# Kernel tuning notes

Hardware: AMD Instinct MI355X
Metric: run time of the kernel (lower is better)

Reference implementation:

```python
import jax, jax.numpy as jnp
import numpy as np

DIM = 512
HEADS = 8
DIM_HEAD = 64  # dim // 8
LANDMARKS = 256  # dim // 2
PINV_ITERS = 6
CONV_K = 33  # residual_conv_kernel default in nystrom-attention
SCALE = DIM_HEAD ** -0.5


def setup_inputs() -> dict:
    key = jax.random.key(0)
    ks = jax.random.split(key, 6)
    B, N = 4, 4096
    inner = HEADS * DIM_HEAD  # 512
    x = jax.random.normal(ks[0], (B, N, DIM), dtype=jnp.float32)
    gamma = jnp.ones((DIM,), jnp.float32)
    beta = jnp.zeros((DIM,), jnp.float32)
    w_qkv = jax.random.normal(ks[1], (DIM, 3 * inner), jnp.float32) * 0.02
    w_out = jax.random.normal(ks[2], (inner, DIM), jnp.float32) * 0.02
    b_out = jnp.zeros((DIM,), jnp.float32)
    # depthwise Conv2d(heads, heads, (33,1), groups=heads, bias=False): OIHW = (H,1,33,1)
    conv_w = jax.random.normal(ks[3], (HEADS, 1, CONV_K, 1), jnp.float32) * 0.1
    return {"x": x, "gamma": gamma, "beta": beta, "w_qkv": w_qkv,
            "w_out": w_out, "b_out": b_out, "conv_w": conv_w}


def _layernorm(x, gamma, beta, eps=1e-5):
    mu = x.mean(-1, keepdims=True)
    var = ((x - mu) ** 2).mean(-1, keepdims=True)
    return (x - mu) * jax.lax.rsqrt(var + eps) * gamma + beta


def _pinv_newton_schulz(a, iters=PINV_ITERS):
    # Moore-Penrose pseudo-inverse via iterative scheme (lucidrains)
    abs_a = jnp.abs(a)
    col = abs_a.sum(-1).max()  # global scalar max, as torch.max
    row = abs_a.sum(-2).max()
    z = jnp.swapaxes(a, -1, -2) / (col * row)
    I = jnp.eye(a.shape[-1], dtype=a.dtype)
    for _ in range(iters):
        az = a @ z
        z = 0.25 * z @ (13. * I - az @ (15. * I - az @ (7. * I - az)))
    return z


def reference(x, gamma, beta, w_qkv, w_out, b_out, conv_w):
    B, N, _ = x.shape
    m = LANDMARKS
    l = N // m  # N chosen divisible by m, so no padding branch
    xn = _layernorm(x, gamma, beta)
    qkv = xn @ w_qkv  # [B,N,3*inner]
    q, k, v = jnp.split(qkv, 3, axis=-1)
    # [B,H,N,D]
    def split_heads(t):
        return t.reshape(B, N, HEADS, DIM_HEAD).transpose(0, 2, 1, 3)
    q, k, v = split_heads(q) * SCALE, split_heads(k), split_heads(v)
    # landmarks: mean over contiguous groups of l tokens -> [B,H,m,D]
    q_l = q.reshape(B, HEADS, m, l, DIM_HEAD).mean(3)
    k_l = k.reshape(B, HEADS, m, l, DIM_HEAD).mean(3)
    attn1 = jax.nn.softmax(jnp.einsum('bhid,bhjd->bhij', q, k_l), axis=-1)    # [B,H,N,m]
    attn2 = jax.nn.softmax(jnp.einsum('bhid,bhjd->bhij', q_l, k_l), axis=-1)  # [B,H,m,m]
    attn3 = jax.nn.softmax(jnp.einsum('bhid,bhjd->bhij', q_l, k), axis=-1)    # [B,H,m,N]
    attn2_inv = _pinv_newton_schulz(attn2)
    out = (attn1 @ attn2_inv) @ (attn3 @ v)  # [B,H,N,D]
    # residual depthwise conv over sequence dim, per head (channels=heads)
    out = out + jax.lax.conv_general_dilated(
        v, conv_w, window_strides=(1, 1),
        padding=[(CONV_K // 2, CONV_K // 2), (0, 0)],
        dimension_numbers=('NCHW', 'OIHW', 'NCHW'),
        feature_group_count=HEADS)
    out = out.transpose(0, 2, 1, 3).reshape(B, N, HEADS * DIM_HEAD)
    attn_out = out @ w_out + b_out  # dropout is identity at eval
    return x + attn_out
```

## Files before the change

### kernel.cpp

```cpp
#include <hip/hip_runtime.h>
#include <math.h>

#define BH 32
#define N_ 4096
#define D_ 64
#define M_ 256
#define L_ 16
#define DIM_ 512
#define K3_ 1536

typedef __attribute__((ext_vector_type(4))) float f32x4;
typedef __attribute__((ext_vector_type(8))) short s16x8;
typedef unsigned short ushort_t;

__device__ inline ushort_t f2bf(float f){
  union{float f; unsigned u;} v; v.f = f;
  unsigned r = v.u + 0x7fffu + ((v.u >> 16) & 1u);
  return (ushort_t)(r >> 16);
}
__device__ inline float bf2f(ushort_t b){
  union{unsigned u; float f;} v; v.u = ((unsigned)b) << 16; return v.f;
}

__device__ inline void gl_lds16(const ushort_t* g, ushort_t* l){
  __builtin_amdgcn_global_load_lds(
      (const __attribute__((address_space(1))) unsigned int*)g,
      (__attribute__((address_space(3))) unsigned int*)l, 16, 0, 0);
}

__device__ inline int xcd_swz_bid(){
  int bid = blockIdx.x + gridDim.x*(blockIdx.y + gridDim.y*blockIdx.z);
  int nwg = gridDim.x*gridDim.y*gridDim.z;
  int cpx = nwg >> 3;
  return (bid & 7)*cpx + (bid >> 3);
}

__device__ inline float wave_sum(float v){
  #pragma unroll
  for (int o=32;o;o>>=1) v += __shfl_down(v,o,64);
  return v;
}
__device__ inline float wave_max(float v){
  #pragma unroll
  for (int o=32;o;o>>=1) v = fmaxf(v,__shfl_down(v,o,64));
  return v;
}
__device__ inline float blk_sum256(float v, float* sm){
  v = wave_sum(v);
  int lane = threadIdx.x & 63, wid = threadIdx.x >> 6;
  if (lane==0) sm[wid]=v;
  __syncthreads();
  float r = sm[0]+sm[1]+sm[2]+sm[3];
  __syncthreads();
  return r;
}
__device__ inline float blk_max256(float v, float* sm){
  v = wave_max(v);
  int lane = threadIdx.x & 63, wid = threadIdx.x >> 6;
  if (lane==0) sm[wid]=v;
  __syncthreads();
  float r = fmaxf(fmaxf(sm[0],sm[1]),fmaxf(sm[2],sm[3]));
  __syncthreads();
  return r;
}

__global__ __launch_bounds__(256) void ln_k(const float* __restrict__ x,
    const float* __restrict__ g, const float* __restrict__ bt, ushort_t* __restrict__ xn){
  int row = blockIdx.x, t = threadIdx.x;
  __shared__ float sm[4];
  const float* xr = x + (size_t)row*DIM_;
  float v0 = xr[t], v1 = xr[t+256];
  float mu = blk_sum256(v0+v1, sm) * (1.f/DIM_);
  float d0 = v0-mu, d1 = v1-mu;
  float var = blk_sum256(d0*d0+d1*d1, sm) * (1.f/DIM_);
  float rs = rsqrtf(var + 1e-5f);
  ushort_t* xo = xn + (size_t)row*DIM_;
  xo[t]     = f2bf(d0*rs*g[t]     + bt[t]);
  xo[t+256] = f2bf(d1*rs*g[t+256] + bt[t+256]);
}

__global__ __launch_bounds__(256) void twb_k(const float* __restrict__ src,
    ushort_t* __restrict__ dst, int R, int C){
  __shared__ ushort_t tile[64][66];
  size_t boff = (size_t)blockIdx.z * R * C;
  int r0 = blockIdx.y*64, c0 = blockIdx.x*64;
  int t = threadIdx.x, c = t & 63, r4 = t >> 6;
  #pragma unroll
  for (int i=0;i<16;i++){
    int rr = r4 + i*4;
    tile[c][rr] = f2bf(src[boff + (size_t)(r0+rr)*C + (c0+c)]);
  }
  __syncthreads();
  #pragma unroll
  for (int i=0;i<16;i++){
    int cc = r4 + i*4;
    dst[boff + (size_t)(c0+cc)*R + (r0 + c)] = tile[cc][c];
  }
}
__global__ __launch_bounds__(256) void tbb_k(const ushort_t* __restrict__ src,
    ushort_t* __restrict__ dst, int R, int C){
  __shared__ ushort_t tile[64][66];
  size_t boff = (size_t)blockIdx.z * R * C;
  int r0 = blockIdx.y*64, c0 = blockIdx.x*64;
  int t = threadIdx.x, c = t & 63, r4 = t >> 6;
  #pragma unroll
  for (int i=0;i<16;i++){
    int rr = r4 + i*4;
    tile[c][rr] = src[boff + (size_t)(r0+rr)*C + (c0+c)];
  }
  __syncthreads();
  #pragma unroll
  for (int i=0;i<16;i++){
    int cc = r4 + i*4;
    dst[boff + (size_t)(c0+cc)*R + (r0 + c)] = tile[cc][c];
  }
}

__global__ __launch_bounds__(256) void gemm_qkv_k(const ushort_t* __restrict__ A,
    const ushort_t* __restrict__ Bt, ushort_t* __restrict__ qb, ushort_t* __restrict__ kb,
    ushort_t* __restrict__ vb){
  __shared__ __align__(16) ushort_t As[128*64];
  __shared__ __align__(16) ushort_t Bs[128*64];
  int t = threadIdx.x;
  int lane = t & 63, wave = t >> 6;
  int l16 = lane & 15, quad = lane >> 4;
  int wm = (wave & 1) * 64, wn = (wave >> 1) * 64;
  int swz = xcd_swz_bid();
  int bx = swz % gridDim.x, by = swz / gridDim.x;
  int row0 = by * 128, col0 = bx * 128;
  f32x4 acc[4][4];
  #pragma unroll
  for (int i=0;i<4;i++)
    #pragma unroll
    for (int j=0;j<4;j++) acc[i][j] = (f32x4){0.f,0.f,0.f,0.f};
  int lr = lane >> 3, lc = lane & 7;
  int scol = (lc ^ lr) * 8;
  int rx7 = l16 & 7;
  for (int k0=0;k0<DIM_;k0+=64){
    __syncthreads();
    #pragma unroll
    for (int p=0;p<4;p++){
      int r = wave*8 + p*32;
      gl_lds16(&A [(size_t)(row0+r+lr)*DIM_ + k0 + scol], &As[(size_t)r*64]);
      gl_lds16(&Bt[(size_t)(col0+r+lr)*DIM_ + k0 + scol], &Bs[(size_t)r*64]);
    }
    __syncthreads();
    s16x8 af[4][2], bf[4][2];
    #pragma unroll
    for (int mt=0;mt<4;mt++)
      #pragma unroll
      for (int kk=0;kk<2;kk++)
        af[mt][kk] = *(const s16x8*)&As[(wm + mt*16 + l16)*64 + (((kk*4+quad)^rx7)*8)];
    #pragma unroll
    for (int nt=0;nt<4;nt++)
      #pragma unroll
      for (int kk=0;kk<2;kk++)
        bf[nt][kk] = *(const s16x8*)&Bs[(wn + nt*16 + l16)*64 + (((kk*4+quad)^rx7)*8)];
    #pragma unroll
    for (int mt=0;mt<4;mt++)
      #pragma unroll
      for (int nt=0;nt<4;nt++)
        #pragma unroll
        for (int kk=0;kk<2;kk++)
          acc[mt][nt] = __builtin_amdgcn_mfma_f32_16x16x32_bf16(af[mt][kk], bf[nt][kk], acc[mt][nt], 0,0,0);
  }
  #pragma unroll
  for (int mt=0;mt<4;mt++){
    #pragma unroll
    for (int nt=0;nt<4;nt++){
      #pragma unroll
      for (int reg=0;reg<4;reg++){
        int row = row0 + wm + mt*16 + quad*4 + reg;
        int col = col0 + wn + nt*16 + l16;
        float val = acc[mt][nt][reg];
        int b = row >> 12, n = row & 4095;
        int which = col >> 9, rem = col & 511;
        int h = rem >> 6, d = rem & 63;
        size_t dst = ((size_t)((b<<3)+h)*N_ + n)*D_ + d;
        if (which==0)      qb[dst] = f2bf(val*0.125f);
        else if (which==1) kb[dst] = f2bf(val);
        else               vb[dst] = f2bf(val);
      }
    }
  }
}

__global__ __launch_bounds__(256) void final3_k(const ushort_t* __restrict__ A,
    const ushort_t* __restrict__ Bt, const float* __restrict__ bo,
    const float* __restrict__ x, float* __restrict__ y){
  __shared__ __align__(16) ushort_t As[128*64];
  __shared__ __align__(16) ushort_t Bs[64*64];
  int t = threadIdx.x;
  int lane = t & 63, wave = t >> 6;
  int l16 = lane & 15, quad = lane >> 4;
  int wm = wave * 32;
  int swz = xcd_swz_bid();
  int bx = swz % gridDim.x, by = swz / gridDim.x;
  int row0 = by * 128, col0 = bx * 64;
  f32x4 acc[2][4];
  #pragma unroll
  for (int i=0;i<2;i++)
    #pragma unroll
    for (int j=0;j<4;j++) acc[i][j] = (f32x4){0.f,0.f,0.f,0.f};
  int lr = lane >> 3, lc = lane & 7;
  int scol = (lc ^ lr) * 8;
  int rx7 = l16 & 7;
  for (int k0=0;k0<DIM_;k0+=64){
    __syncthreads();
    #pragma unroll
    for (int p=0;p<4;p++){
      int r = wave*8 + p*32;
      gl_lds16(&A[(size_t)(row0+r+lr)*DIM_ + k0 + scol], &As[(size_t)r*64]);
    }
    #pragma unroll
    for (int p=0;p<2;p++){
      int r = wave*8 + p*32;
      gl_lds16(&Bt[(size_t)(col0+r+lr)*DIM_ + k0 + scol], &Bs[(size_t)r*64]);
    }
    __syncthreads();
    s16x8 af[2][2], bf[4][2];
    #pragma unroll
    for (int mt=0;mt<2;mt++)
      #pragma unroll
      for (int kk=0;kk<2;kk++)
        af[mt][kk] = *(const s16x8*)&As[(wm + mt*16 + l16)*64 + (((kk*4+quad)^rx7)*8)];
    #pragma unroll
    for (int nt=0;nt<4;nt++)
      #pragma unroll
      for (int kk=0;kk<2;kk++)
        bf[nt][kk] = *(const s16x8*)&Bs[(nt*16 + l16)*64 + (((kk*4+quad)^rx7)*8)];
    #pragma unroll
    for (int mt=0;mt<2;mt++)
      #pragma unroll
      for (int nt=0;nt<4;nt++)
        #pragma unroll
        for (int kk=0;kk<2;kk++)
          acc[mt][nt] = __builtin_amdgcn_mfma_f32_16x16x32_bf16(af[mt][kk], bf[nt][kk], acc[mt][nt], 0,0,0);
  }
  #pragma unroll
  for (int mt=0;mt<2;mt++){
    #pragma unroll
    for (int nt=0;nt<4;nt++){
      int col = col0 + nt*16 + l16;
      #pragma unroll
      for (int reg=0;reg<4;reg++){
        int row = row0 + wm + mt*16 + quad*4 + reg;
        size_t o = (size_t)row*DIM_ + col;
        y[o] = acc[mt][nt][reg] + bo[col] + x[o];
      }
    }
  }
}

__global__ void lmk_k(const ushort_t* __restrict__ q, const ushort_t* __restrict__ k,
                      float* __restrict__ ql, float* __restrict__ kl,
                      ushort_t* __restrict__ qlh, ushort_t* __restrict__ qll,
                      ushort_t* __restrict__ klh, ushort_t* __restrict__ kll){
  int idx = blockIdx.x*256 + threadIdx.x;
  int d = idx & 63, i = (idx >> 6) & 255, bh = idx >> 14;
  size_t base = ((size_t)bh*N_ + i*L_)*D_ + d;
  float sq=0.f, sk=0.f;
  #pragma unroll
  for (int tt=0;tt<L_;tt++){ sq += bf2f(q[base + (size_t)tt*D_]); sk += bf2f(k[base + (size_t)tt*D_]); }
  sq *= (1.f/L_); sk *= (1.f/L_);
  ql[idx] = sq; kl[idx] = sk;
  ushort_t qh = f2bf(sq), kh = f2bf(sk);
  qlh[idx] = qh; qll[idx] = f2bf(sq - bf2f(qh));
  klh[idx] = kh; kll[idx] = f2bf(sk - bf2f(kh));
}

__global__ __launch_bounds__(256) void attn2m_k(
    const ushort_t* __restrict__ qlh, const ushort_t* __restrict__ qll,
    const ushort_t* __restrict__ klh, const ushort_t* __restrict__ kll,
    float* __restrict__ a2f, ushort_t* __restrict__ a2h, ushort_t* __restrict__ a2l,
    float* __restrict__ cs, float* __restrict__ rs){
  int bh = blockIdx.y;
  int t = threadIdx.x, wave = t >> 6, lane = t & 63;
  int l16 = lane & 15, quad = lane >> 4;
  size_t mo = (size_t)bh*M_*M_;
  int rowtile = blockIdx.x*32 + wave*16;
  size_t qbase = ((size_t)bh*M_ + rowtile + l16)*D_;
  s16x8 qh0 = *(const s16x8*)&qlh[qbase + quad*8];
  s16x8 qh1 = *(const s16x8*)&qlh[qbase + 32 + quad*8];
  s16x8 qv0 = *(const s16x8*)&qll[qbase + quad*8];
  s16x8 qv1 = *(const s16x8*)&qll[qbase + 32 + quad*8];
  f32x4 s[16];
  #pragma unroll
  for (int kt=0;kt<16;kt++){
    size_t kb = ((size_t)bh*M_ + kt*16 + l16)*D_;
    s16x8 kh0 = *(const s16x8*)&klh[kb + quad*8];
    s16x8 kh1 = *(const s16x8*)&klh[kb + 32 + quad*8];
    s16x8 kv0 = *(const s16x8*)&kll[kb + quad*8];
    s16x8 kv1 = *(const s16x8*)&kll[kb + 32 + quad*8];
    f32x4 z = (f32x4){0.f,0.f,0.f,0.f};
    z = __builtin_amdgcn_mfma_f32_16x16x32_bf16(qh0, kh0, z, 0,0,0);
    z = __builtin_amdgcn_mfma_f32_16x16x32_bf16(qh1, kh1, z, 0,0,0);
    z = __builtin_amdgcn_mfma_f32_16x16x32_bf16(qh0, kv0, z, 0,0,0);
    z = __builtin_amdgcn_mfma_f32_16x16x32_bf16(qh1, kv1, z, 0,0,0);
    z = __builtin_amdgcn_mfma_f32_16x16x32_bf16(qv0, kh0, z, 0,0,0);
    z = __builtin_amdgcn_mfma_f32_16x16x32_bf16(qv1, kh1, z, 0,0,0);
    s[kt] = z;
  }
  float mx[4], inv[4];
  #pragma unroll
  for (int r=0;r<4;r++){
    float m = s[0][r];
    #pragma unroll
    for (int kt=1;kt<16;kt++) m = fmaxf(m, s[kt][r]);
    m = fmaxf(m, __shfl_xor(m, 1));
    m = fmaxf(m, __shfl_xor(m, 2));
    m = fmaxf(m, __shfl_xor(m, 4));
    m = fmaxf(m, __shfl_xor(m, 8));
    mx[r] = m;
  }
  float lsum[4] = {0.f,0.f,0.f,0.f};
  #pragma unroll
  for (int kt=0;kt<16;kt++){
    #pragma unroll
    for (int r=0;r<4;r++){
      float e = expf(s[kt][r] - mx[r]);
      s[kt][r] = e;
      lsum[r] += e;
    }
  }
  #pragma unroll
  for (int r=0;r<4;r++){
    float ls = lsum[r];
    ls += __shfl_xor(ls, 1);
    ls += __shfl_xor(ls, 2);
    ls += __shfl_xor(ls, 4);
    ls += __shfl_xor(ls, 8);
    inv[r] = 1.f/ls;
  }
  if (l16 == 0){
    #pragma unroll
    for (int r=0;r<4;r++) rs[(size_t)bh*M_ + rowtile + quad*4 + r] = 1.0f;
  }
  #pragma unroll
  for (int kt=0;kt<16;kt++){
    int c = kt*16 + l16;
    float csum = 0.f;
    #pragma unroll
    for (int r=0;r<4;r++){
      float p = s[kt][r]*inv[r];
      csum += p;
      size_t oi = mo + (size_t)(rowtile + quad*4 + r)*M_ + c;
      a2f[oi] = p;
      ushort_t hh = f2bf(p);
      a2h[oi] = hh;
      a2l[oi] = f2bf(p - bf2f(hh));
    }
    csum += __shfl_xor(csum, 16);
    csum += __shfl_xor(csum, 32);
    if (lane < 16) atomicAdd(&cs[(size_t)bh*M_ + c], csum);
  }
}

__global__ __launch_bounds__(256) void maxred_k(const float* __restrict__ cs,
    const float* __restrict__ rs, float* __restrict__ scal){
  __shared__ float sm[4];
  float cm=-1e30f, rm=-1e30f;
  for (int i=threadIdx.x;i<BH*M_;i+=256){ cm=fmaxf(cm,cs[i]); rm=fmaxf(rm,rs[i]); }
  cm = blk_max256(cm, sm);
  rm = blk_max256(rm, sm);
  if (threadIdx.x==0) scal[0] = 1.f/(cm*rm);
}

__global__ __launch_bounds__(256) void initz3_k(const float* __restrict__ a2,
    const float* __restrict__ scal,
    ushort_t* __restrict__ zh, ushort_t* __restrict__ zl,
    ushort_t* __restrict__ zTh, ushort_t* __restrict__ zTl){
  __shared__ float tile[64][65];
  int bh = blockIdx.z;
  size_t mo = (size_t)bh*M_*M_;
  float s = scal[0];
  int r0 = blockIdx.y*64, c0 = blockIdx.x*64;
  int t = threadIdx.x, c = t & 63, r4 = t >> 6;
  #pragma unroll
  for (int i=0;i<16;i++){
    int rr = r4 + i*4;
    float v = a2[mo + (size_t)(r0+rr)*M_ + c0 + c] * s;
    tile[rr][c] = v;
    ushort_t hh = f2bf(v);
    size_t oi = mo + (size_t)(r0+rr)*M_ + c0 + c;
    zTh[oi] = hh;
    zTl[oi] = f2bf(v - bf2f(hh));
  }
  __syncthreads();
  #pragma unroll
  for (int i=0;i<16;i++){
    int zr = r4 + i*4;
    float v = tile[c][zr];
    size_t oi = mo + (size_t)(c0+zr)*M_ + r0 + c;
    ushort_t hh = f2bf(v);
    zh[oi] = hh;
    zl[oi] = f2bf(v - bf2f(hh));
  }
}

template<bool HASCOEF, bool WN, bool WT, bool WF>
__global__ __launch_bounds__(256) void ns3_k(
    const ushort_t* __restrict__ Ah, const ushort_t* __restrict__ Al,
    const ushort_t* __restrict__ BTh, const ushort_t* __restrict__ BTl,
    float coef, float scale,
    ushort_t* __restrict__ Ch, ushort_t* __restrict__ Cl,
    ushort_t* __restrict__ CTh, ushort_t* __restrict__ CTl,
    float* __restrict__ Cf){
  __shared__ __align__(16) ushort_t Ahs[64*64];
  __shared__ __align__(16) ushort_t Als[64*64];
  __shared__ __align__(16) ushort_t Bhs[64*64];
  __shared__ __align__(16) ushort_t Bls[64*64];
  int swz = xcd_swz_bid();
  int bx = swz % gridDim.x; int rem = swz / gridDim.x;
  int by = rem % gridDim.y; int batch = rem / gridDim.y;
  size_t mo = (size_t)batch*M_*M_;
  int row0 = by*64, col0 = bx*64;
  int t = threadIdx.x, lane = t & 63, wave = t >> 6;
  int l16 = lane & 15, quad = lane >> 4;
  f32x4 acc[4];
  #pragma unroll
  for (int j=0;j<4;j++) acc[j] = (f32x4){0.f,0.f,0.f,0.f};
  int lr = lane >> 3, lc = lane & 7;
  int scol = (lc ^ lr) * 8;
  int rx7 = l16 & 7;
  for (int k0=0;k0<M_;k0+=64){
    __syncthreads();
    #pragma unroll
    for (int p=0;p<2;p++){
      int r = wave*8 + p*32;
      gl_lds16(&Ah [mo + (size_t)(row0+r+lr)*M_ + k0 + scol], &Ahs[(size_t)r*64]);
      gl_lds16(&Al [mo + (size_t)(row0+r+lr)*M_ + k0 + scol], &Als[(size_t)r*64]);
      gl_lds16(&BTh[mo + (size_t)(col0+r+lr)*M_ + k0 + scol], &Bhs[(size_t)r*64]);
      gl_lds16(&BTl[mo + (size_t)(col0+r+lr)*M_ + k0 + scol], &Bls[(size_t)r*64]);
    }
    __syncthreads();
    s16x8 fah[2], fal[2];
    #pragma unroll
    for (int kk=0;kk<2;kk++){
      fah[kk] = *(const s16x8*)&Ahs[(wave*16 + l16)*64 + (((kk*4+quad)^rx7)*8)];
      fal[kk] = *(const s16x8*)&Als[(wave*16 + l16)*64 + (((kk*4+quad)^rx7)*8)];
    }
    #pragma unroll
    for (int nt=0;nt<4;nt++){
      #pragma unroll
      for (int kk=0;kk<2;kk++){
        s16x8 fbh = *(const s16x8*)&Bhs[(nt*16 + l16)*64 + (((kk*4+quad)^rx7)*8)];
        s16x8 fbl = *(const s16x8*)&Bls[(nt*16 + l16)*64 + (((kk*4+quad)^rx7)*8)];
        acc[nt] = __builtin_amdgcn_mfma_f32_16x16x32_bf16(fah[kk], fbh, acc[nt], 0,0,0);
        acc[nt] = __builtin_amdgcn_mfma_f32_16x16x32_bf16(fah[kk], fbl, acc[nt], 0,0,0);
        acc[nt] = __builtin_amdgcn_mfma_f32_16x16x32_bf16(fal[kk], fbh, acc[nt], 0,0,0);
      }
    }
  }
  int rbase = row0 + wave*16 + quad*4;
  #pragma unroll
  for (int nt=0;nt<4;nt++){
    int c = col0 + nt*16 + l16;
    ushort_t th[4], tl[4];
    #pragma unroll
    for (int reg=0;reg<4;reg++){
      float a = acc[nt][reg];
      float base = 0.f;
      if (HASCOEF){
        size_t ai = mo + (size_t)(rbase+reg)*M_ + c;
        base = coef*(bf2f(Ah[ai]) + bf2f(Al[ai]));
      }
      float v = scale*(base - a);
      if (WF) Cf[mo + (size_t)(rbase+reg)*M_ + c] = v;
      ushort_t hh = f2bf(v);
      ushort_t ll = f2bf(v - bf2f(hh));
      if (WN){
        Ch[mo + (size_t)(rbase+reg)*M_ + c] = hh;
        Cl[mo + (size_t)(rbase+reg)*M_ + c] = ll;
      }
      th[reg] = hh; tl[reg] = ll;
    }
    if (WT){
      uint2 vh; vh.x = (unsigned)th[0] | ((unsigned)th[1]<<16); vh.y = (unsigned)th[2] | ((unsigned)th[3]<<16);
      uint2 vl; vl.x = (unsigned)tl[0] | ((unsigned)tl[1]<<16); vl.y = (unsigned)tl[2] | ((unsigned)tl[3]<<16);
      *(uint2*)&CTh[mo + (size_t)c*M_ + rbase] = vh;
      *(uint2*)&CTl[mo + (size_t)c*M_ + rbase] = vl;
    }
  }
}

template<int ITERS, bool SCATTER>
__global__ __launch_bounds__(256) void attn7_k(const ushort_t* __restrict__ Q,
    const ushort_t* __restrict__ K, const ushort_t* __restrict__ VT,
    int nq, int nk,
    float* __restrict__ up, float* __restrict__ mst, float* __restrict__ lst,
    ushort_t* __restrict__ ob){
  __shared__ __align__(16) ushort_t Ks[64*72];
  __shared__ __align__(16) ushort_t Vs[64*72];
  __shared__ __align__(16) ushort_t Pb[4*16*76];
  int swz = xcd_swz_bid();
  int qblk = swz % gridDim.x; int rem0 = swz / gridDim.x;
  int half = rem0 % gridDim.y; int bh = rem0 / gridDim.y;
  int key0 = half * (ITERS*64);
  int t = threadIdx.x, wave = t >> 6, lane = t & 63;
  int l16 = lane & 15, quad = lane >> 4;
  size_t qbase = ((size_t)bh*nq + qblk*64 + wave*16 + l16)*D_;
  s16x8 qa0 = *(const s16x8*)&Q[qbase + quad*8];
  s16x8 qa1 = *(const s16x8*)&Q[qbase + 32 + quad*8];
  const ushort_t* Kb = K + (size_t)bh*nk*D_;
  const ushort_t* Vb = VT + (size_t)bh*D_*nk;
  ushort_t* Pw = &Pb[wave*16*76];
  float m_j = -1e30f, l_j = 0.f;
  f32x4 oacc[4];
  #pragma unroll
  for (int d=0;d<4;d++) oacc[d] = (f32x4){0.f,0.f,0.f,0.f};
  for (int it=0; it<ITERS; it++){
    int j0 = key0 + it*64;
    __syncthreads();
    #pragma unroll
    for (int p=0;p<2;p++){
      int idx = t + p*256;
      int kr = idx >> 3, kc = (idx & 7)*8;
      *(uint4*)&Ks[kr*72 + kc] = *(const uint4*)&Kb[(size_t)(j0+kr)*D_ + kc];
      *(uint4*)&Vs[kr*72 + kc] = *(const uint4*)&Vb[(size_t)kr*nk + j0 + kc];
    }
    __syncthreads();
    f32x4 st[4];
    #pragma unroll
    for (int kt=0;kt<4;kt++){
      s16x8 b0 = *(const s16x8*)&Ks[(kt*16 + l16)*72 + quad*8];
      s16x8 b1 = *(const s16x8*)&Ks[(kt*16 + l16)*72 + 32 + quad*8];
      f32x4 z = (f32x4){0.f,0.f,0.f,0.f};
      z = __builtin_amdgcn_mfma_f32_16x16x32_bf16(b0, qa0, z, 0,0,0);
      z = __builtin_amdgcn_mfma_f32_16x16x32_bf16(b1, qa1, z, 0,0,0);
      st[kt] = z;
    }
    float mx = st[0][0];
    #pragma unroll
    for (int kt=0;kt<4;kt++)
      #pragma unroll
      for (int r=0;r<4;r++) mx = fmaxf(mx, st[kt][r]);
    mx = fmaxf(mx, __shfl_xor(mx, 16));
    mx = fmaxf(mx, __shfl_xor(mx, 32));
    float mn = fmaxf(m_j, mx);
    float alpha = __expf(m_j - mn);
    m_j = mn;
    float lsum = 0.f;
    #pragma unroll
    for (int kt=0;kt<4;kt++){
      ushort_t pk[4];
      #pragma unroll
      for (int r=0;r<4;r++){
        float p = __expf(st[kt][r] - mn);
        lsum += p;
        pk[r] = f2bf(p);
      }
      uint2 w;
      w.x = (unsigned)pk[0] | ((unsigned)pk[1] << 16);
      w.y = (unsigned)pk[2] | ((unsigned)pk[3] << 16);
      *(uint2*)&Pw[l16*76 + kt*16 + quad*4] = w;
    }
    lsum += __shfl_xor(lsum, 16);
    lsum += __shfl_xor(lsum, 32);
    l_j = l_j*alpha + lsum;
    float ab[4];
    #pragma unroll
    for (int r=0;r<4;r++) ab[r] = __shfl(alpha, quad*4 + r, 64);
    #pragma unroll
    for (int d=0;d<4;d++)
      #pragma unroll
      for (int r=0;r<4;r++) oacc[d][r] *= ab[r];
    #pragma unroll
    for (int ks=0;ks<2;ks++){
      s16x8 pa = *(const s16x8*)&Pw[l16*76 + ks*32 + quad*8];
      #pragma unroll
      for (int dt=0;dt<4;dt++){
        s16x8 vv = *(const s16x8*)&Vs[(dt*16 + l16)*72 + ks*32 + quad*8];
        oacc[dt] = __builtin_amdgcn_mfma_f32_16x16x32_bf16(pa, vv, oacc[dt], 0,0,0);
      }
    }
  }
  int rowbase = qblk*64 + wave*16 + quad*4;
  if (SCATTER){
    float lb[4];
    #pragma unroll
    for (int r=0;r<4;r++) lb[r] = __shfl(l_j, quad*4 + r, 64);
    int b = bh >> 3, h = bh & 7;
    #pragma unroll
    for (int dt=0;dt<4;dt++){
      #pragma unroll
      for (int r=0;r<4;r++){
        int n = rowbase + r;
        ob[((size_t)(b*N_ + n))*DIM_ + h*D_ + dt*16 + l16] = f2bf(oacc[dt][r] / lb[r]);
      }
    }
  } else {
    size_t pb = ((size_t)(half*BH + bh)*M_ + rowbase)*D_;
    #pragma unroll
    for (int dt=0;dt<4;dt++){
      #pragma unroll
      for (int r=0;r<4;r++)
        up[pb + (size_t)r*D_ + dt*16 + l16] = oacc[dt][r];
    }
    if (lane < 16){
      size_t si = (size_t)(half*BH + bh)*M_ + qblk*64 + wave*16 + l16;
      mst[si] = m_j;
      lst[si] = l_j;
    }
  }
}

__global__ __launch_bounds__(256) void comb_k(const float* __restrict__ up,
    const float* __restrict__ mst, const float* __restrict__ lst,
    float* __restrict__ u){
  int idx = blockIdx.x*256 + threadIdx.x;
  int d = idx & 63; int row = (idx >> 6) & 255; int bh = idx >> 14;
  float m = -1e30f;
  float mv[8];
  #pragma unroll
  for (int hfs=0;hfs<8;hfs++){
    mv[hfs] = mst[(size_t)(hfs*BH + bh)*M_ + row];
    m = fmaxf(m, mv[hfs]);
  }
  float num = 0.f, den = 0.f;
  #pragma unroll
  for (int hfs=0;hfs<8;hfs++){
    float w = __expf(mv[hfs] - m);
    size_t ri = (size_t)(hfs*BH + bh)*M_ + row;
    den += lst[ri] * w;
    num += up[ri*D_ + d] * w;
  }
  u[idx] = num / den;
}

__global__ void zu_k(const float* __restrict__ z, const float* __restrict__ u,
                     float* __restrict__ w){
  int idx = blockIdx.x*256 + threadIdx.x;
  int d = idx & 63, i = (idx >> 6) & 255, bh = idx >> 14;
  const float* zr = z + ((size_t)bh*M_+i)*M_;
  const float* ub = u + (size_t)bh*M_*D_ + d;
  float acc = 0.f;
  for (int kk=0;kk<M_;kk++) acc += zr[kk]*ub[(size_t)kk*D_];
  w[idx] = acc;
}

__global__ __launch_bounds__(256) void conv3_k(const ushort_t* __restrict__ v,
    const float* __restrict__ cw, ushort_t* __restrict__ ob){
  int bh = blockIdx.y;
  int h = bh & 7, b = bh >> 3;
  int t = threadIdx.x;
  int d8 = (t & 7) * 8;
  int nloc = t >> 3;
  int n0 = blockIdx.x * 128 + nloc * 4;
  __shared__ float wsm[33];
  if (t < 33) wsm[t] = cw[h*33 + t];
  __syncthreads();
  float acc[4][8];
  #pragma unroll
  for (int j=0;j<4;j++)
    #pragma unroll
    for (int dd=0;dd<8;dd++) acc[j][dd] = 0.f;
  const ushort_t* vbase = v + (size_t)bh*N_*D_;
  for (int r=0;r<36;r++){
    int nn = n0 - 16 + r;
    float vals[8];
    if (nn >= 0 && nn < N_){
      uint4 raw = *(const uint4*)&vbase[(size_t)nn*D_ + d8];
      const ushort_t* pr = (const ushort_t*)&raw;
      #pragma unroll
      for (int dd=0;dd<8;dd++) vals[dd] = bf2f(pr[dd]);
    } else {
      #pragma unroll
      for (int dd=0;dd<8;dd++) vals[dd] = 0.f;
    }
    #pragma unroll
    for (int j=0;j<4;j++){
      int tap = r - j;
      if (tap >= 0 && tap <= 32){
        float wj = wsm[tap];
        #pragma unroll
        for (int dd=0;dd<8;dd++) acc[j][dd] += wj * vals[dd];
      }
    }
  }
  #pragma unroll
  for (int j=0;j<4;j++){
    size_t oi = ((size_t)(b*N_ + n0 + j))*DIM_ + h*D_ + d8;
    uint4 cur = *(uint4*)&ob[oi];
    ushort_t* pc = (ushort_t*)&cur;
    #pragma unroll
    for (int dd=0;dd<8;dd++) pc[dd] = f2bf(bf2f(pc[dd]) + acc[j][dd]);
    *(uint4*)&ob[oi] = cur;
  }
}

extern "C" void kernel_launch(void* const* d_in, const int* in_sizes, int n_in,
                              void* d_out, int out_size, void* d_ws, size_t ws_size,
                              hipStream_t stream){
  (void)in_sizes; (void)n_in; (void)out_size; (void)ws_size;
  const float* x      = (const float*)d_in[0];
  const float* gamma  = (const float*)d_in[1];
  const float* beta   = (const float*)d_in[2];
  const float* w_qkv  = (const float*)d_in[3];
  const float* w_out  = (const float*)d_in[4];
  const float* b_out  = (const float*)d_in[5];
  const float* conv_w = (const float*)d_in[6];
  float* y = (float*)d_out;
  float* ws = (float*)d_ws;

  size_t off = 0;
  ushort_t* xnb   = (ushort_t*)(ws + off); off += 4194304;
  ushort_t* qb    = (ushort_t*)(ws + off); off += 4194304;
  ushort_t* kb    = (ushort_t*)(ws + off); off += 4194304;
  ushort_t* vb    = (ushort_t*)(ws + off); off += 4194304;
  ushort_t* vT    = (ushort_t*)(ws + off); off += 4194304;
  ushort_t* wqkvT = (ushort_t*)(ws + off); off += 393216;
  ushort_t* woutT = (ushort_t*)(ws + off); off += 131072;
  ushort_t* qlh   = (ushort_t*)(ws + off); off += 262144;
  ushort_t* qll   = (ushort_t*)(ws + off); off += 262144;
  ushort_t* klh   = (ushort_t*)(ws + off); off += 262144;
  ushort_t* kll   = (ushort_t*)(ws + off); off += 262144;
  ushort_t* wzT   = (ushort_t*)(ws + off); off += 262144;
  ushort_t* ob    = (ushort_t*)(ws + off); off += 4194304;
  ushort_t* a2h   = (ushort_t*)(ws + off); off += 1048576;
  ushort_t* a2l   = (ushort_t*)(ws + off); off += 1048576;
  ushort_t* z0h   = (ushort_t*)(ws + off); off += 1048576;
  ushort_t* z0l   = (ushort_t*)(ws + off); off += 1048576;
  ushort_t* z0Th  = (ushort_t*)(ws + off); off += 1048576;
  ushort_t* z0Tl  = (ushort_t*)(ws + off); off += 1048576;
  ushort_t* z1h   = (ushort_t*)(ws + off); off += 1048576;
  ushort_t* z1l   = (ushort_t*)(ws + off); off += 1048576;
  ushort_t* z1Th  = (ushort_t*)(ws + off); off += 1048576;
  ushort_t* z1Tl  = (ushort_t*)(ws + off); off += 1048576;
  ushort_t* t1Th  = (ushort_t*)(ws + off); off += 1048576;
  ushort_t* t1Tl  = (ushort_t*)(ws + off); off += 1048576;
  ushort_t* t2Th  = (ushort_t*)(ws + off); off += 1048576;
  ushort_t* t2Tl  = (ushort_t*)(ws + off); off += 1048576;
  float* ql  = ws + off;  off += 524288;
  float* kl  = ws + off;  off += 524288;
  float* a2f = ws + off;  off += 2097152;
  float* zf  = ws + off;  off += 2097152;
  float* u   = ws + off;  off += 524288;
  float* wz  = ws + off;  off += 524288;
  float* up  = ws + off;  off += 4194304;
  float* mstat = ws + off; off += 65536;
  float* lstat = ws + off; off += 65536;
  float* cs  = ws + off;  off += 8192;
  float* rs  = ws + off;  off += 8192;
  float* scal = ws + off; off += 8;
  ushort_t* azh  = xnb;
  ushort_t* azl  = xnb + 2097152;
  ushort_t* azTh = xnb + 2*2097152;
  ushort_t* azTl = xnb + 3*2097152;

  hipMemsetAsync(cs, 0, BH*M_*sizeof(float), stream);
  ln_k<<<16384,256,0,stream>>>(x, gamma, beta, xnb);
  twb_k<<<dim3(24,8,1),256,0,stream>>>(w_qkv, wqkvT, 512, 1536);
  twb_k<<<dim3(8,8,1),256,0,stream>>>(w_out, woutT, 512, 512);
  gemm_qkv_k<<<dim3(12,128),256,0,stream>>>(xnb, wqkvT, qb, kb, vb);
  tbb_k<<<dim3(1,64,32),256,0,stream>>>(vb, vT, 4096, 64);
  lmk_k<<<2048,256,0,stream>>>(qb, kb, ql, kl, qlh, qll, klh, kll);
  attn2m_k<<<dim3(8,32),128,0,stream>>>(qlh, qll, klh, kll, a2f, a2h, a2l, cs, rs);
  maxred_k<<<1,256,0,stream>>>(cs, rs, scal);
  initz3_k<<<dim3(4,4,32),256,0,stream>>>(a2f, scal, z0h, z0l, z0Th, z0Tl);

  ushort_t *zch = z0h, *zcl = z0l, *zcTh = z0Th, *zcTl = z0Tl;
  ushort_t *znh = z1h, *znl = z1l, *znTh = z1Th, *znTl = z1Tl;
  dim3 nsg(4,4,32);
  for (int it=0; it<6; it++){
    ns3_k<false,true,true,false><<<nsg,256,0,stream>>>(a2h, a2l, zcTh, zcTl,
        0.f, -1.f, azh, azl, azTh, azTl, (float*)nullptr);
    ns3_k<true,false,true,false><<<nsg,256,0,stream>>>(azh, azl, azTh, azTl,
        7.f, 1.f, (ushort_t*)nullptr, (ushort_t*)nullptr, t1Th, t1Tl, (float*)nullptr);
    ns3_k<true,false,true,false><<<nsg,256,0,stream>>>(azh, azl, t1Th, t1Tl,
        15.f, 1.f, (ushort_t*)nullptr, (ushort_t*)nullptr, t2Th, t2Tl, (float*)nullptr);
    if (it < 5)
      ns3_k<true,true,true,false><<<nsg,256,0,stream>>>(zch, zcl, t2Th, t2Tl,
          13.f, 0.25f, znh, znl, znTh, znTl, (float*)nullptr);
    else
      ns3_k<true,true,true,true><<<nsg,256,0,stream>>>(zch, zcl, t2Th, t2Tl,
          13.f, 0.25f, znh, znl, znTh, znTl, zf);
    { ushort_t* tp;
      tp=zch; zch=znh; znh=tp;  tp=zcl; zcl=znl; znl=tp;
      tp=zcTh; zcTh=znTh; znTh=tp;  tp=zcTl; zcTl=znTl; znTl=tp; }
  }

  attn7_k<8,false><<<dim3(4,8,32),256,0,stream>>>(qlh, kb, vT, M_, N_,
      up, mstat, lstat, (ushort_t*)nullptr);
  comb_k<<<2048,256,0,stream>>>(up, mstat, lstat, u);
  zu_k<<<2048,256,0,stream>>>(zf, u, wz);
  twb_k<<<dim3(1,4,32),256,0,stream>>>(wz, wzT, 256, 64);
  attn7_k<4,true><<<dim3(64,1,32),256,0,stream>>>(qb, klh, wzT, N_, M_,
      (float*)nullptr, (float*)nullptr, (float*)nullptr, ob);
  conv3_k<<<dim3(32,32),256,0,stream>>>(vb, conv_w, ob);
  final3_k<<<dim3(8,128),256,0,stream>>>(ob, woutT, b_out, x, y);
}
```

Measured before the change: 553.2 us.

## Use wave-per-row layernorm and direct-to-LDS swizzled loads in attention kernels

```diff
diff --git a/kernel.cpp b/kernel.cpp
--- a/kernel.cpp
+++ b/kernel.cpp
@@ -40,19 +40,15 @@
   for (int o=32;o;o>>=1) v += __shfl_down(v,o,64);
   return v;
 }
+__device__ inline float wave_sum_all(float v){
+  #pragma unroll
+  for (int o=1;o<64;o<<=1) v += __shfl_xor(v,o,64);
+  return v;
+}
 __device__ inline float wave_max(float v){
   #pragma unroll
   for (int o=32;o;o>>=1) v = fmaxf(v,__shfl_down(v,o,64));
   return v;
-}
-__device__ inline float blk_sum256(float v, float* sm){
-  v = wave_sum(v);
-  int lane = threadIdx.x & 63, wid = threadIdx.x >> 6;
-  if (lane==0) sm[wid]=v;
-  __syncthreads();
-  float r = sm[0]+sm[1]+sm[2]+sm[3];
-  __syncthreads();
-  return r;
 }
 __device__ inline float blk_max256(float v, float* sm){
   v = wave_max(v);
@@ -64,19 +60,32 @@
   return r;
 }
 
-__global__ __launch_bounds__(256) void ln_k(const float* __restrict__ x,
+__global__ __launch_bounds__(256) void ln2_k(const float* __restrict__ x,
     const float* __restrict__ g, const float* __restrict__ bt, ushort_t* __restrict__ xn){
-  int row = blockIdx.x, t = threadIdx.x;
-  __shared__ float sm[4];
-  const float* xr = x + (size_t)row*DIM_;
-  float v0 = xr[t], v1 = xr[t+256];
-  float mu = blk_sum256(v0+v1, sm) * (1.f/DIM_);
-  float d0 = v0-mu, d1 = v1-mu;
-  float var = blk_sum256(d0*d0+d1*d1, sm) * (1.f/DIM_);
+  int t = threadIdx.x, lane = t & 63, w = t >> 6;
+  size_t row = (size_t)blockIdx.x*4 + w;
+  const float* xr = x + row*DIM_;
+  f32x4 a = *(const f32x4*)&xr[lane*8];
+  f32x4 b = *(const f32x4*)&xr[lane*8+4];
+  float s = a[0]+a[1]+a[2]+a[3]+b[0]+b[1]+b[2]+b[3];
+  float mu = wave_sum_all(s) * (1.f/DIM_);
+  float d[8];
+  #pragma unroll
+  for (int i=0;i<4;i++){ d[i] = a[i]-mu; d[i+4] = b[i]-mu; }
+  float vs = 0.f;
+  #pragma unroll
+  for (int i=0;i<8;i++) vs += d[i]*d[i];
+  float var = wave_sum_all(vs) * (1.f/DIM_);
   float rs = rsqrtf(var + 1e-5f);
-  ushort_t* xo = xn + (size_t)row*DIM_;
-  xo[t]     = f2bf(d0*rs*g[t]     + bt[t]);
-  xo[t+256] = f2bf(d1*rs*g[t+256] + bt[t+256]);
+  f32x4 g0 = *(const f32x4*)&g[lane*8], g1 = *(const f32x4*)&g[lane*8+4];
+  f32x4 b0 = *(const f32x4*)&bt[lane*8], b1 = *(const f32x4*)&bt[lane*8+4];
+  ushort_t tmp[8];
+  #pragma unroll
+  for (int i=0;i<4;i++){
+    tmp[i]   = f2bf(d[i]*rs*g0[i]   + b0[i]);
+    tmp[i+4] = f2bf(d[i+4]*rs*g1[i] + b1[i]);
+  }
+  *(uint4*)&xn[row*DIM_ + lane*8] = *(uint4*)tmp;
 }
 
 __global__ __launch_bounds__(256) void twb_k(const float* __restrict__ src,
@@ -485,13 +494,13 @@
 }
 
 template<int ITERS, bool SCATTER>
-__global__ __launch_bounds__(256) void attn7_k(const ushort_t* __restrict__ Q,
+__global__ __launch_bounds__(256) void attn8_k(const ushort_t* __restrict__ Q,
     const ushort_t* __restrict__ K, const ushort_t* __restrict__ VT,
     int nq, int nk,
     float* __restrict__ up, float* __restrict__ mst, float* __restrict__ lst,
     ushort_t* __restrict__ ob){
-  __shared__ __align__(16) ushort_t Ks[64*72];
-  __shared__ __align__(16) ushort_t Vs[64*72];
+  __shared__ __align__(16) ushort_t Ks[64*64];
+  __shared__ __align__(16) ushort_t Vs[64*64];
   __shared__ __align__(16) ushort_t Pb[4*16*76];
   int swz = xcd_swz_bid();
   int qblk = swz % gridDim.x; int rem0 = swz / gridDim.x;
@@ -505,6 +514,9 @@
   const ushort_t* Kb = K + (size_t)bh*nk*D_;
   const ushort_t* Vb = VT + (size_t)bh*D_*nk;
   ushort_t* Pw = &Pb[wave*16*76];
+  int lr = lane >> 3, lc = lane & 7;
+  int scol = (lc ^ lr) * 8;
+  int rx7 = l16 & 7;
   float m_j = -1e30f, l_j = 0.f;
   f32x4 oacc[4];
   #pragma unroll
@@ -514,17 +526,16 @@
     __syncthreads();
     #pragma unroll
     for (int p=0;p<2;p++){
-      int idx = t + p*256;
-      int kr = idx >> 3, kc = (idx & 7)*8;
-      *(uint4*)&Ks[kr*72 + kc] = *(const uint4*)&Kb[(size_t)(j0+kr)*D_ + kc];
-      *(uint4*)&Vs[kr*72 + kc] = *(const uint4*)&Vb[(size_t)kr*nk + j0 + kc];
+      int r = wave*8 + p*32;
+      gl_lds16(&Kb[(size_t)(j0+r+lr)*D_ + scol], &Ks[(size_t)r*64]);
+      gl_lds16(&Vb[(size_t)(r+lr)*nk + j0 + scol], &Vs[(size_t)r*64]);
     }
     __syncthreads();
     f32x4 st[4];
     #pragma unroll
     for (int kt=0;kt<4;kt++){
-      s16x8 b0 = *(const s16x8*)&Ks[(kt*16 + l16)*72 + quad*8];
-      s16x8 b1 = *(const s16x8*)&Ks[(kt*16 + l16)*72 + 32 + quad*8];
+      s16x8 b0 = *(const s16x8*)&Ks[(kt*16 + l16)*64 + ((quad^rx7)*8)];
+      s16x8 b1 = *(const s16x8*)&Ks[(kt*16 + l16)*64 + (((4+quad)^rx7)*8)];
       f32x4 z = (f32x4){0.f,0.f,0.f,0.f};
       z = __builtin_amdgcn_mfma_f32_16x16x32_bf16(b0, qa0, z, 0,0,0);
       z = __builtin_amdgcn_mfma_f32_16x16x32_bf16(b1, qa1, z, 0,0,0);
@@ -570,7 +581,7 @@
       s16x8 pa = *(const s16x8*)&Pw[l16*76 + ks*32 + quad*8];
       #pragma unroll
       for (int dt=0;dt<4;dt++){
-        s16x8 vv = *(const s16x8*)&Vs[(dt*16 + l16)*72 + ks*32 + quad*8];
+        s16x8 vv = *(const s16x8*)&Vs[(dt*16 + l16)*64 + (((ks*4+quad)^rx7)*8)];
         oacc[dt] = __builtin_amdgcn_mfma_f32_16x16x32_bf16(pa, vv, oacc[dt], 0,0,0);
       }
     }
@@ -749,7 +760,7 @@
   ushort_t* azTl = xnb + 3*2097152;
 
   hipMemsetAsync(cs, 0, BH*M_*sizeof(float), stream);
-  ln_k<<<16384,256,0,stream>>>(x, gamma, beta, xnb);
+  ln2_k<<<4096,256,0,stream>>>(x, gamma, beta, xnb);
   twb_k<<<dim3(24,8,1),256,0,stream>>>(w_qkv, wqkvT, 512, 1536);
   twb_k<<<dim3(8,8,1),256,0,stream>>>(w_out, woutT, 512, 512);
   gemm_qkv_k<<<dim3(12,128),256,0,stream>>>(xnb, wqkvT, qb, kb, vb);
@@ -780,12 +791,12 @@
       tp=zcTh; zcTh=znTh; znTh=tp;  tp=zcTl; zcTl=znTl; znTl=tp; }
   }
 
-  attn7_k<8,false><<<dim3(4,8,32),256,0,stream>>>(qlh, kb, vT, M_, N_,
+  attn8_k<8,false><<<dim3(4,8,32),256,0,stream>>>(qlh, kb, vT, M_, N_,
       up, mstat, lstat, (ushort_t*)nullptr);
   comb_k<<<2048,256,0,stream>>>(up, mstat, lstat, u);
   zu_k<<<2048,256,0,stream>>>(zf, u, wz);
   twb_k<<<dim3(1,4,32),256,0,stream>>>(wz, wzT, 256, 64);
-  attn7_k<4,true><<<dim3(64,1,32),256,0,stream>>>(qb, klh, wzT, N_, M_,
+  attn8_k<4,true><<<dim3(64,1,32),256,0,stream>>>(qb, klh, wzT, N_, M_,
       (float*)nullptr, (float*)nullptr, (float*)nullptr, ob);
   conv3_k<<<dim3(32,32),256,0,stream>>>(vb, conv_w, ob);
   final3_k<<<dim3(8,128),256,0,stream>>>(ob, woutT, b_out, x, y);
```

New measurement: 543.5 us. About the same (-1.7%).
